# Optimization experiments

Measured on AMD Instinct MI355X. Metric: run time of the kernel, lower is better.

## Reference

```python
import jax, jax.numpy as jnp
import numpy as np


def setup_inputs() -> dict:
    key = jax.random.key(0)
    k1, k2, k3, k4 = jax.random.split(key, 4)
    B, C, T = 32, 512, 1024
    N, D = 64, 512
    scale = 1.0 / np.sqrt(C)
    x = jax.random.normal(k1, (B, C, T), dtype=jnp.float32)
    subjects = jax.random.randint(k2, (B,), 0, N, dtype=jnp.int64)
    weights = jax.random.normal(k3, (N, C, D), dtype=jnp.float32) * scale
    bias = jax.random.normal(k4, (N, D), dtype=jnp.float32) * scale
    return {"x": x, "subjects": subjects, "weights": weights, "bias": bias}


def reference(x, subjects, weights, bias):
    # gather mode: per-example projection matrix, then batched GEMM
    # x: (B, C, T); weights[subjects]: (B, C, D) -> out: (B, D, T)
    w = weights[subjects]                      # (B, C, D)
    out = jnp.einsum('bct,bcd->bdt', x, w)
    out = out + bias[subjects][:, :, None]     # (B, D, 1) broadcast over T
    return out
```

## Files before the change

### kernel.cpp

```cpp
#include <hip/hip_runtime.h>
#include <hip/hip_bf16.h>

#define B_N 32
#define C_K 512
#define T_N 1024
#define D_M 512

constexpr int BM = 128, BN = 128, BK = 32;
constexpr int SA = 40;
constexpr int KSTEPS = C_K / BK;

typedef __attribute__((ext_vector_type(4))) float  floatx4;
typedef __attribute__((ext_vector_type(8))) short  shortx8;
typedef __attribute__((ext_vector_type(4))) unsigned int uintx4;

__device__ __forceinline__ unsigned pk2(float a, float b) {
  __hip_bfloat162 h = __float22bfloat162_rn(make_float2(a, b));
  union { __hip_bfloat162 v; unsigned u; } c; c.v = h; return c.u;
}

__global__ __launch_bounds__(256, 3)
void subject_gemm(const float* __restrict__ x, const int* __restrict__ subjects,
                  const float* __restrict__ weights, const float* __restrict__ bias,
                  float* __restrict__ out)
{
  __shared__ __align__(16) short lds_a[2][BM * SA];
  __shared__ __align__(16) short lds_b[2][BN * SA];

  const int bid  = blockIdx.x;
  const int xcd  = bid & 7;
  const int s    = bid >> 3;
  const int b    = xcd * 4 + (s & 3);
  const int tile = s >> 2;
  const int tm = tile >> 3, tn = tile & 7;
  const int m0 = tm * BM, n0 = tn * BN;
  const int nb = subjects[b];

  const float* __restrict__ Wp = weights + (size_t)nb * C_K * D_M;
  const float* __restrict__ Xp = x + (size_t)b * C_K * T_N;

  const int tid  = threadIdx.x;
  const int lane = tid & 63;
  const int wave = tid >> 6;

  const bool isA = (wave < 2);
  const int  mg  = (wave & 1) * 16 + (lane & 15);
  const int  oct = lane >> 4;
  const float* gsrc = isA ? (Wp + (size_t)(8 * oct) * D_M + (m0 + 4 * mg))
                          : (Xp + (size_t)(8 * oct) * T_N + (n0 + 4 * mg));
  const int gs = isA ? D_M : T_N;
  const int sw   = (mg >> 2) & 3;
  const int cOff = 8 * (oct ^ sw);
  short* const wbase = (isA ? &lds_a[0][0] : &lds_b[0][0]) + (4 * mg) * SA + cOff;
  constexpr int BUFO = BM * SA;

  const int wm = (wave & 1) * 64, wn = (wave >> 1) * 64;
  const int l15 = lane & 15, q = lane >> 4;

  floatx4 acc[4][4] = {};
  floatx4 v[8];

  #pragma unroll
  for (int jj = 0; jj < 8; ++jj)
    v[jj] = *(const floatx4*)(gsrc + (size_t)jj * gs);
  gsrc += (size_t)BK * gs;
  #pragma unroll
  for (int r = 0; r < 4; ++r) {
    uintx4 pk = { pk2(v[0][r], v[1][r]), pk2(v[2][r], v[3][r]),
                  pk2(v[4][r], v[5][r]), pk2(v[6][r], v[7][r]) };
    *(uintx4*)(wbase + r * SA) = pk;
  }

  for (int ks = 0; ks < KSTEPS; ++ks) {
    const int p = ks & 1;
    __syncthreads();

    if (ks + 1 < KSTEPS) {
      #pragma unroll
      for (int jj = 0; jj < 8; ++jj)
        v[jj] = *(const floatx4*)(gsrc + (size_t)jj * gs);
      gsrc += (size_t)BK * gs;
    }

    const short* pa = &lds_a[p][0] + (wm + l15) * SA;
    const short* pb = &lds_b[p][0] + (wn + l15) * SA;
    shortx8 af[4], bg[4];
    #pragma unroll
    for (int i = 0; i < 4; ++i) {
      af[i] = *(const shortx8*)(pa + 16 * i * SA + 8 * (q ^ i));
      bg[i] = *(const shortx8*)(pb + 16 * i * SA + 8 * (q ^ i));
    }
    #pragma unroll
    for (int i = 0; i < 4; ++i)
      #pragma unroll
      for (int j = 0; j < 4; ++j)
        acc[i][j] = __builtin_amdgcn_mfma_f32_16x16x32_bf16(af[i], bg[j], acc[i][j], 0, 0, 0);

    if (ks + 1 < KSTEPS) {
      short* wdst = wbase + (p ^ 1) * BUFO;
      #pragma unroll
      for (int r = 0; r < 4; ++r) {
        uintx4 pk = { pk2(v[0][r], v[1][r]), pk2(v[2][r], v[3][r]),
                      pk2(v[4][r], v[5][r]), pk2(v[6][r], v[7][r]) };
        *(uintx4*)(wdst + r * SA) = pk;
      }
    }
  }

  float* __restrict__ O = out + (size_t)b * D_M * T_N;
  const float* __restrict__ bb = bias + (size_t)nb * D_M;
  #pragma unroll
  for (int i = 0; i < 4; ++i) {
    #pragma unroll
    for (int r = 0; r < 4; ++r) {
      const int d = m0 + wm + 16 * i + 4 * q + r;
      const float bv = bb[d];
      #pragma unroll
      for (int j = 0; j < 4; ++j) {
        const int t = n0 + wn + 16 * j + l15;
        O[(size_t)d * T_N + t] = acc[i][j][r] + bv;
      }
    }
  }
}

extern "C" void kernel_launch(void* const* d_in, const int* in_sizes, int n_in,
                              void* d_out, int out_size, void* d_ws, size_t ws_size,
                              hipStream_t stream) {
  const float* x        = (const float*)d_in[0];
  const int*   subjects = (const int*)d_in[1];
  const float* weights  = (const float*)d_in[2];
  const float* bias     = (const float*)d_in[3];
  float* out = (float*)d_out;
  (void)in_sizes; (void)n_in; (void)out_size; (void)d_ws; (void)ws_size;

  dim3 grid(B_N * 4 * 8);
  dim3 block(256);
  hipLaunchKernelGGL(subject_gemm, grid, block, 0, stream, x, subjects, weights, bias, out);
}
```

Before: 178.0 us.

## Deepen global-load prefetch by one stage and use a lighter barrier

Result: slower. 188.4 us (+5.9%).

```diff
diff --git a/kernel.cpp b/kernel.cpp
--- a/kernel.cpp
+++ b/kernel.cpp
@@ -7,7 +7,7 @@
 #define D_M 512
 
 constexpr int BM = 128, BN = 128, BK = 32;
-constexpr int SA = 40;
+constexpr int SA = 32;
 constexpr int KSTEPS = C_K / BK;
 
 typedef __attribute__((ext_vector_type(4))) float  floatx4;
@@ -17,6 +17,12 @@
 __device__ __forceinline__ unsigned pk2(float a, float b) {
   __hip_bfloat162 h = __float22bfloat162_rn(make_float2(a, b));
   union { __hip_bfloat162 v; unsigned u; } c; c.v = h; return c.u;
+}
+
+__device__ __forceinline__ void wg_barrier() {
+  asm volatile("s_waitcnt lgkmcnt(0)" ::: "memory");
+  __builtin_amdgcn_s_barrier();
+  __builtin_amdgcn_sched_barrier(0);
 }
 
 __global__ __launch_bounds__(256, 3)
@@ -60,27 +66,29 @@
   floatx4 acc[4][4] = {};
   floatx4 v[8];
 
-  #pragma unroll
-  for (int jj = 0; jj < 8; ++jj)
-    v[jj] = *(const floatx4*)(gsrc + (size_t)jj * gs);
-  gsrc += (size_t)BK * gs;
-  #pragma unroll
-  for (int r = 0; r < 4; ++r) {
-    uintx4 pk = { pk2(v[0][r], v[1][r]), pk2(v[2][r], v[3][r]),
-                  pk2(v[4][r], v[5][r]), pk2(v[6][r], v[7][r]) };
-    *(uintx4*)(wbase + r * SA) = pk;
-  }
+  auto loads = [&]() {
+    #pragma unroll
+    for (int jj = 0; jj < 8; ++jj)
+      v[jj] = *(const floatx4*)(gsrc + (size_t)jj * gs);
+    gsrc += (size_t)BK * gs;
+  };
+  auto cvt_store = [&](int p) {
+    short* wdst = wbase + p * BUFO;
+    #pragma unroll
+    for (int r = 0; r < 4; ++r) {
+      uintx4 pk = { pk2(v[0][r], v[1][r]), pk2(v[2][r], v[3][r]),
+                    pk2(v[4][r], v[5][r]), pk2(v[6][r], v[7][r]) };
+      *(uintx4*)(wdst + r * SA) = pk;
+    }
+  };
+
+  loads();
+  cvt_store(0);
+  loads();
 
   for (int ks = 0; ks < KSTEPS; ++ks) {
     const int p = ks & 1;
-    __syncthreads();
-
-    if (ks + 1 < KSTEPS) {
-      #pragma unroll
-      for (int jj = 0; jj < 8; ++jj)
-        v[jj] = *(const floatx4*)(gsrc + (size_t)jj * gs);
-      gsrc += (size_t)BK * gs;
-    }
+    wg_barrier();
 
     const short* pa = &lds_a[p][0] + (wm + l15) * SA;
     const short* pb = &lds_b[p][0] + (wn + l15) * SA;
@@ -96,15 +104,8 @@
       for (int j = 0; j < 4; ++j)
         acc[i][j] = __builtin_amdgcn_mfma_f32_16x16x32_bf16(af[i], bg[j], acc[i][j], 0, 0, 0);
 
-    if (ks + 1 < KSTEPS) {
-      short* wdst = wbase + (p ^ 1) * BUFO;
-      #pragma unroll
-      for (int r = 0; r < 4; ++r) {
-        uintx4 pk = { pk2(v[0][r], v[1][r]), pk2(v[2][r], v[3][r]),
-                      pk2(v[4][r], v[5][r]), pk2(v[6][r], v[7][r]) };
-        *(uintx4*)(wdst + r * SA) = pk;
-      }
-    }
+    if (ks + 1 < KSTEPS) cvt_store(p ^ 1);
+    if (ks + 2 < KSTEPS) loads();
   }
 
   float* __restrict__ O = out + (size_t)b * D_M * T_N;
```
